# Kernel optimization log

Measured on AMD Instinct MI355X. Metric: run time of the kernel, lower is better.

Reference implementation:

```python
import jax, jax.numpy as jnp
import numpy as np

N_NODES = 20000
N_EDGES = 160000
N_GRAPHS = 64
DIMS = [9, 128, 256, 512, 1534]
NEG_SLOPE_ATT = 0.2   # GATConv attention LeakyReLU
NEG_SLOPE_ACT = 0.01  # nn.LeakyReLU between layers
EPS = 1e-5            # GraphNorm eps


def setup_inputs() -> dict:
    key = jax.random.key(0)
    inp = {}
    k, key = jax.random.split(key)
    inp['x'] = jax.random.normal(k, (N_NODES, DIMS[0]), jnp.float32)
    k, key = jax.random.split(key)
    inp['edge_index'] = jax.random.randint(k, (2, N_EDGES), 0, N_NODES)
    k, key = jax.random.split(key)
    inp['batch'] = jnp.sort(jax.random.randint(k, (N_NODES,), 0, N_GRAPHS))
    for l in range(4):
        din, dout = DIMS[l], DIMS[l + 1]
        k1, k2, k3, key = jax.random.split(key, 4)
        s = 1.0 / np.sqrt(din)
        inp[f'W{l}'] = (jax.random.normal(k1, (din, dout)) * s).astype(jnp.float32)
        inp[f'asrc{l}'] = (jax.random.normal(k2, (dout,)) * 0.1).astype(jnp.float32)
        inp[f'adst{l}'] = (jax.random.normal(k3, (dout,)) * 0.1).astype(jnp.float32)
        inp[f'b{l}'] = jnp.zeros((dout,), jnp.float32)
        inp[f'g{l}'] = jnp.ones((dout,), jnp.float32)   # GraphNorm weight
        inp[f'bt{l}'] = jnp.zeros((dout,), jnp.float32)  # GraphNorm bias
        inp[f'ms{l}'] = jnp.ones((dout,), jnp.float32)   # GraphNorm mean_scale
    return inp


def _gat_conv(h, src, dst, n, W, asrc, adst, b):
    # PyG GATConv, heads=1: linear (no bias), edge attention, segment softmax, scatter-add
    hp = h @ W                                                    # [N, dout]
    e = jax.nn.leaky_relu((hp @ asrc)[src] + (hp @ adst)[dst], NEG_SLOPE_ATT)  # [E]
    m = jax.ops.segment_max(e, dst, num_segments=n)
    m = jnp.where(jnp.isfinite(m), m, 0.0)
    ex = jnp.exp(e - m[dst])
    denom = jax.ops.segment_sum(ex, dst, num_segments=n)
    alpha = ex / (denom[dst] + 1e-16)                             # [E]
    out = jax.ops.segment_sum(alpha[:, None] * hp[src], dst, num_segments=n)
    return out + b


def _graph_norm(h, batch, counts, g, bt, ms):
    # PyG GraphNorm: per-graph mean/var with learnable mean_scale
    mean = jax.ops.segment_sum(h, batch, num_segments=N_GRAPHS) / counts
    out = h - ms * mean[batch]
    var = jax.ops.segment_sum(out * out, batch, num_segments=N_GRAPHS) / counts
    return out / jnp.sqrt(var[batch] + EPS) * g + bt


def _forward(x, edge_index, batch, params):
    n = x.shape[0]
    loops = jnp.arange(n)
    src = jnp.concatenate([edge_index[0], loops])   # GATConv add_self_loops=True
    dst = jnp.concatenate([edge_index[1], loops])
    counts = jax.ops.segment_sum(jnp.ones((n,), x.dtype), batch, num_segments=N_GRAPHS)[:, None]
    h = x
    for (W, asrc, adst, b, g, bt, ms) in params:
        h = _gat_conv(h, src, dst, n, W, asrc, adst, b)
        h = jax.nn.leaky_relu(h, NEG_SLOPE_ACT)
        h = _graph_norm(h, batch, counts, g, bt, ms)
        # Dropout(p=0.1) is identity in eval mode
    mean = (jax.ops.segment_sum(h, batch, num_segments=N_GRAPHS) / counts)[:, None, :]
    mx = jax.ops.segment_max(h, batch, num_segments=N_GRAPHS)[:, None, :]
    return jnp.concatenate([mean, mx], axis=1)      # [G, 2, 1534]


def reference(x, edge_index, batch,
              W0, asrc0, adst0, b0, g0, bt0, ms0,
              W1, asrc1, adst1, b1, g1, bt1, ms1,
              W2, asrc2, adst2, b2, g2, bt2, ms2,
              W3, asrc3, adst3, b3, g3, bt3, ms3):
    params = [
        (W0, asrc0, adst0, b0, g0, bt0, ms0),
        (W1, asrc1, adst1, b1, g1, bt1, ms1),
        (W2, asrc2, adst2, b2, g2, bt2, ms2),
        (W3, asrc3, adst3, b3, g3, bt3, ms3),
    ]
    return _forward(x, edge_index, batch, params)
```

## Files before the change

### kernel.cpp

```cpp
#include <hip/hip_runtime.h>
#include <math.h>

typedef unsigned int u32;
typedef unsigned short u16;
using half8 = __attribute__((ext_vector_type(8))) _Float16;
using f32x4 = __attribute__((ext_vector_type(4))) float;

#define NN 20000
#define MPAD 20096
#define NE 160000
#define ET 180000
#define NG 64
#define NBLK 79

constexpr float NEG_ATT = 0.2f;
constexpr float NEG_ACT = 0.01f;
constexpr float EPS_GN  = 1e-5f;

struct Ptr4 { const float *p0, *p1, *p2, *p3; };


__device__ __forceinline__ u16 f2h(float f) {
    _Float16 h = (_Float16)f;
    return __builtin_bit_cast(u16, h);
}
__device__ __forceinline__ float h2f(u16 b) {
    return (float)__builtin_bit_cast(_Float16, b);
}

__device__ __forceinline__ void gl_lds16(const void* g, void* l) {
    __builtin_amdgcn_global_load_lds((const __attribute__((address_space(1))) u32*)g,
                                     (__attribute__((address_space(3))) u32*)l, 16, 0, 0);
}

__device__ __forceinline__ float lrelu_att(float v) {
    return (v > 0.f) ? v : NEG_ATT * v;
}


__global__ void k_bounds(const int* __restrict__ batch, int* __restrict__ counts,
                         int* __restrict__ gstart) {
    __shared__ int ls[NG + 1];
    int g = threadIdx.x;
    int lo = 0, hi = NN;
    while (lo < hi) {
        int mid = (lo + hi) >> 1;
        if (batch[mid] < g) lo = mid + 1; else hi = mid;
    }
    ls[g] = lo;
    if (g == 0) ls[NG] = NN;
    __syncthreads();
    counts[g] = ls[g + 1] - ls[g];
    gstart[g] = ls[g];
    if (g == 0) gstart[NG] = NN;
}


__global__ void k_deg(const int* __restrict__ ei, int* deg) {
    int i = blockIdx.x * 256 + threadIdx.x;
    if (i >= ET) return;
    int dst = (i < NE) ? ei[NE + i] : (i - NE);
    atomicAdd(&deg[dst], 1);
}

__global__ void k_scan1(const int* __restrict__ deg, int* __restrict__ bsum) {
    int i = blockIdx.x * 256 + threadIdx.x;
    int v = (i < NN) ? deg[i] : 0;
    int lane = threadIdx.x & 63, w = threadIdx.x >> 6;
    #pragma unroll
    for (int off = 32; off; off >>= 1) v += __shfl_down(v, off, 64);
    __shared__ int ws[4];
    if (lane == 0) ws[w] = v;
    __syncthreads();
    if (threadIdx.x == 0) bsum[blockIdx.x] = ws[0] + ws[1] + ws[2] + ws[3];
}

__global__ void k_scan2(const int* __restrict__ bsum, int* __restrict__ boff,
                        int* __restrict__ total) {
    int tid = threadIdx.x;
    int v = (tid < NBLK) ? bsum[tid] : 0;
    int lane = tid & 63, w = tid >> 6;
    int val = v;
    #pragma unroll
    for (int off = 1; off < 64; off <<= 1) {
        int t = __shfl_up(val, off, 64);
        if (lane >= off) val += t;
    }
    __shared__ int ws[4];
    if (lane == 63) ws[w] = val;
    __syncthreads();
    int woff = 0;
    for (int k = 0; k < w; k++) woff += ws[k];
    int excl = woff + val - v;
    if (tid < NBLK) boff[tid] = excl;
    if (tid == NBLK - 1) *total = excl + v;
}

__global__ void k_scan3(const int* __restrict__ deg, const int* __restrict__ boff,
                        int* __restrict__ row_ptr, int* __restrict__ cursor) {
    int i = blockIdx.x * 256 + threadIdx.x;
    int v = (i < NN) ? deg[i] : 0;
    int lane = threadIdx.x & 63, w = threadIdx.x >> 6;
    int val = v;
    #pragma unroll
    for (int off = 1; off < 64; off <<= 1) {
        int t = __shfl_up(val, off, 64);
        if (lane >= off) val += t;
    }
    __shared__ int ws[4];
    if (lane == 63) ws[w] = val;
    __syncthreads();
    int woff = 0;
    for (int k = 0; k < w; k++) woff += ws[k];
    int excl = boff[blockIdx.x] + woff + val - v;
    if (i < NN) { row_ptr[i] = excl; cursor[i] = excl; }
}

__global__ void k_scatter(const int* __restrict__ ei, int* cursor, int* __restrict__ col) {
    int i = blockIdx.x * 256 + threadIdx.x;
    if (i >= ET) return;
    int s, d;
    if (i < NE) { s = ei[i]; d = ei[NE + i]; } else { s = i - NE; d = s; }
    int p = atomicAdd(&cursor[d], 1);
    col[p] = s;
}


__global__ void k_wvec_all(Ptr4 W, Ptr4 As, Ptr4 Ad,
                           float* __restrict__ wsrcA, float* __restrict__ wdstA) {
    const int dins[4]  = {9, 128, 256, 512};
    const int douts[4] = {128, 256, 512, 1534};
    int l = blockIdx.y, k = blockIdx.x;
    if (k >= dins[l]) return;
    const float* Wp = (l == 0) ? W.p0 : (l == 1) ? W.p1 : (l == 2) ? W.p2 : W.p3;
    const float* as = (l == 0) ? As.p0 : (l == 1) ? As.p1 : (l == 2) ? As.p2 : As.p3;
    const float* ad = (l == 0) ? Ad.p0 : (l == 1) ? Ad.p1 : (l == 2) ? Ad.p2 : Ad.p3;
    int NC = douts[l];
    const float* row = Wp + (size_t)k * NC;
    float ss = 0.f, sd = 0.f;
    for (int n = threadIdx.x; n < NC; n += 256) {
        float w = row[n];
        ss += w * as[n];
        sd += w * ad[n];
    }
    __shared__ float ls[8];
    int lane = threadIdx.x & 63, w4 = threadIdx.x >> 6;
    #pragma unroll
    for (int off = 32; off; off >>= 1) {
        ss += __shfl_down(ss, off, 64);
        sd += __shfl_down(sd, off, 64);
    }
    if (lane == 0) { ls[w4] = ss; ls[4 + w4] = sd; }
    __syncthreads();
    if (threadIdx.x == 0) {
        wsrcA[l * 512 + k] = ls[0] + ls[1] + ls[2] + ls[3];
        wdstA[l * 512 + k] = ls[4] + ls[5] + ls[6] + ls[7];
    }
}


__global__ void k_wbt_all(Ptr4 W, u16* __restrict__ WbTall) {
    const int Ks[3] = {128, 256, 512};
    const int NCs[3] = {256, 512, 1534};
    const int Nps[3] = {256, 512, 1536};
    const size_t offs[3] = {0, 256 * 128, 256 * 128 + 512 * 256};
    int l = blockIdx.z;
    int K = Ks[l], NC = NCs[l], Np = Nps[l];
    int n0 = blockIdx.x * 32, k0 = blockIdx.y * 32;
    if (n0 >= Np || k0 >= K) return;
    const float* Wp = (l == 0) ? W.p1 : (l == 1) ? W.p2 : W.p3;
    u16* WbT = WbTall + offs[l];
    __shared__ u16 tile[32][33];
    int tx = threadIdx.x & 31, ty = threadIdx.x >> 5;
    #pragma unroll
    for (int i = 0; i < 4; i++) {
        int k = k0 + ty + i * 8, n = n0 + tx;
        float v = (k < K && n < NC) ? Wp[(size_t)k * NC + n] : 0.f;
        tile[ty + i * 8][tx] = f2h(v);
    }
    __syncthreads();
    #pragma unroll
    for (int i = 0; i < 4; i++) {
        int n = n0 + ty + i * 8, k = k0 + tx;
        if (n < Np && k < K) WbT[(size_t)n * K + k] = tile[tx][ty + i * 8];
    }
}


__global__ void k_scores0(const float* __restrict__ x, const float* __restrict__ wsrc,
                          const float* __restrict__ wdst, float* __restrict__ s_src,
                          float* __restrict__ s_dst) {
    int v = blockIdx.x * 256 + threadIdx.x;
    if (v >= NN) return;
    const float* r = x + (size_t)v * 9;
    float ss = 0.f, sd = 0.f;
    #pragma unroll
    for (int k = 0; k < 9; k++) { ss += r[k] * wsrc[k]; sd += r[k] * wdst[k]; }
    s_src[v] = ss; s_dst[v] = sd;
}

template <int VW>
__global__ void k_scores_h(const u16* __restrict__ h, const float* __restrict__ wsrc,
                           const float* __restrict__ wdst, float* __restrict__ s_src,
                           float* __restrict__ s_dst, int din) {
    int v = blockIdx.x * 4 + (threadIdx.x >> 6);
    int lane = threadIdx.x & 63;
    if (v >= NN) return;
    const u16* row = h + (size_t)v * din;
    float ss = 0.f, sd = 0.f;
    for (int d = lane * VW; d < din; d += 64 * VW) {
        u32 ua[VW / 2];
        if constexpr (VW == 2) {
            ua[0] = *(const u32*)(row + d);
        } else if constexpr (VW == 4) {
            uint2 t = *(const uint2*)(row + d);
            ua[0] = t.x; ua[1] = t.y;
        } else {
            uint4 t = *(const uint4*)(row + d);
            ua[0] = t.x; ua[1] = t.y; ua[2] = t.z; ua[3] = t.w;
        }
        #pragma unroll
        for (int j = 0; j < VW / 2; j++) {
            float h0 = h2f((u16)(ua[j] & 0xffffu)), h1 = h2f((u16)(ua[j] >> 16));
            ss += h0 * wsrc[d + 2 * j] + h1 * wsrc[d + 2 * j + 1];
            sd += h0 * wdst[d + 2 * j] + h1 * wdst[d + 2 * j + 1];
        }
    }
    #pragma unroll
    for (int off = 32; off; off >>= 1) {
        ss += __shfl_down(ss, off, 64);
        sd += __shfl_down(sd, off, 64);
    }
    if (lane == 0) { s_src[v] = ss; s_dst[v] = sd; }
}


__global__ __launch_bounds__(256) void k_alpha(const int* __restrict__ row_ptr,
                                               const int* __restrict__ col,
                                               const float* __restrict__ s_src,
                                               const float* __restrict__ s_dst,
                                               float* __restrict__ alpha) {
    int grp = threadIdx.x >> 6;
    int lane = threadIdx.x & 63;
    int v = blockIdx.x * 4 + grp;
    if (v >= NN) return;
    int st = row_ptr[v], en = row_ptr[v + 1];
    float sd = s_dst[v];
    float mx = -INFINITY;
    for (int p = st + lane; p < en; p += 64)
        mx = fmaxf(mx, lrelu_att(s_src[col[p]] + sd));
    #pragma unroll
    for (int off = 32; off; off >>= 1) mx = fmaxf(mx, __shfl_xor(mx, off, 64));
    float sum = 0.f;
    for (int p = st + lane; p < en; p += 64)
        sum += __expf(lrelu_att(s_src[col[p]] + sd) - mx);
    #pragma unroll
    for (int off = 32; off; off >>= 1) sum += __shfl_xor(sum, off, 64);
    float inv = 1.0f / (sum + 1e-16f);
    for (int p = st + lane; p < en; p += 64)
        alpha[p] = __expf(lrelu_att(s_src[col[p]] + sd) - mx) * inv;
}


template <int TPN, int CPT>
__global__ __launch_bounds__(256) void k_agg2(const u16* __restrict__ h,
                                              const int* __restrict__ row_ptr,
                                              const int* __restrict__ col,
                                              const float* __restrict__ alpha,
                                              u16* __restrict__ agg, int din) {
    constexpr int NPB = 256 / TPN;
    int grp = threadIdx.x / TPN;
    int lane = threadIdx.x % TPN;
    int v = blockIdx.x * NPB + grp;
    if (v >= NN) return;
    int st = row_ptr[v], en = row_ptr[v + 1];
    int d0 = lane * 2 * CPT;
    const u16* hb = h + d0;
    float acc[2 * CPT];
    #pragma unroll
    for (int i = 0; i < 2 * CPT; i++) acc[i] = 0.f;

    auto ld = [&](int c, u32* t) {
        if constexpr (CPT == 1) {
            t[0] = *(const u32*)(hb + (size_t)c * din);
        } else if constexpr (CPT == 2) {
            uint2 u = *(const uint2*)(hb + (size_t)c * din);
            t[0] = u.x; t[1] = u.y;
        } else {
            uint4 u = *(const uint4*)(hb + (size_t)c * din);
            t[0] = u.x; t[1] = u.y; t[2] = u.z; t[3] = u.w;
        }
    };

    int p = st;
    for (; p + 4 <= en; p += 4) {
        float aa[4];
        u32 t[4][CPT];
        #pragma unroll
        for (int e = 0; e < 4; e++) {
            int c = col[p + e];
            aa[e] = alpha[p + e];
            ld(c, t[e]);
        }
        #pragma unroll
        for (int e = 0; e < 4; e++)
            #pragma unroll
            for (int j = 0; j < CPT; j++) {
                acc[2 * j]     += aa[e] * h2f((u16)(t[e][j] & 0xffffu));
                acc[2 * j + 1] += aa[e] * h2f((u16)(t[e][j] >> 16));
            }
    }
    for (; p < en; p++) {
        float a = alpha[p];
        u32 t[CPT];
        ld(col[p], t);
        #pragma unroll
        for (int j = 0; j < CPT; j++) {
            acc[2 * j]     += a * h2f((u16)(t[j] & 0xffffu));
            acc[2 * j + 1] += a * h2f((u16)(t[j] >> 16));
        }
    }

    u32 o[CPT];
    #pragma unroll
    for (int j = 0; j < CPT; j++)
        o[j] = (u32)f2h(acc[2 * j]) | ((u32)f2h(acc[2 * j + 1]) << 16);
    if constexpr (CPT == 1) {
        *(u32*)(agg + (size_t)v * din + d0) = o[0];
    } else if constexpr (CPT == 2) {
        uint2 ov; ov.x = o[0]; ov.y = o[1];
        *(uint2*)(agg + (size_t)v * din + d0) = ov;
    } else {
        uint4 ov; ov.x = o[0]; ov.y = o[1]; ov.z = o[2]; ov.w = o[3];
        *(uint4*)(agg + (size_t)v * din + d0) = ov;
    }
}

__global__ __launch_bounds__(256) void k_agg0_fused(const float* __restrict__ x,
                                                    const int* __restrict__ row_ptr,
                                                    const int* __restrict__ col,
                                                    const float* __restrict__ s_src,
                                                    const float* __restrict__ s_dst,
                                                    float* __restrict__ agg0) {
    __shared__ float sm[4 * 2];
    int grp = threadIdx.x >> 6;
    int lane = threadIdx.x & 63;
    int v = blockIdx.x * 4 + grp;
    bool valid = v < NN;
    int st = 0, en = 0;
    float sd = 0.f;
    if (valid) { st = row_ptr[v]; en = row_ptr[v + 1]; sd = s_dst[v]; }
    float mx = -INFINITY;
    if (valid) {
        for (int p = st + lane; p < en; p += 64)
            mx = fmaxf(mx, lrelu_att(s_src[col[p]] + sd));
    }
    #pragma unroll
    for (int off = 32; off; off >>= 1) mx = fmaxf(mx, __shfl_xor(mx, off, 64));
    float sum = 0.f;
    if (valid) {
        for (int p = st + lane; p < en; p += 64)
            sum += __expf(lrelu_att(s_src[col[p]] + sd) - mx);
    }
    #pragma unroll
    for (int off = 32; off; off >>= 1) sum += __shfl_xor(sum, off, 64);
    if (lane == 0) { sm[grp * 2] = mx; sm[grp * 2 + 1] = 1.0f / (sum + 1e-16f); }
    __syncthreads();
    if (!valid || lane >= 9) return;
    float m = sm[grp * 2], inv = sm[grp * 2 + 1];
    float acc = 0.f;
    for (int p = st; p < en; p++) {
        int c = col[p];
        float a = __expf(lrelu_att(s_src[c] + sd) - m);
        acc += a * x[(size_t)c * 9 + lane];
    }
    agg0[(size_t)v * 9 + lane] = acc * inv;
}


__global__ __launch_bounds__(256) void k_gemm0(const float* __restrict__ agg0,
                                               const float* __restrict__ W,
                                               const float* __restrict__ bias,
                                               u16* __restrict__ out) {
    __shared__ float Ws[9 * 128];
    for (int i = threadIdx.x; i < 9 * 128; i += 256) Ws[i] = W[i];
    __syncthreads();
    int node = blockIdx.x * 2 + (threadIdx.x >> 7);
    int n = threadIdx.x & 127;
    if (node >= NN) return;
    const float* xr = agg0 + (size_t)node * 9;
    float acc = bias[n];
    #pragma unroll
    for (int k = 0; k < 9; k++) acc += xr[k] * Ws[k * 128 + n];
    acc = (acc > 0.f) ? acc : NEG_ACT * acc;
    out[(size_t)node * 128 + n] = f2h(acc);
}


#define BM 128
#define BK 32

__global__ __launch_bounds__(256) void k_gemm_f16(const u16* __restrict__ A,
                                                  const u16* __restrict__ B,
                                                  const float* __restrict__ bias,
                                                  u16* __restrict__ C,
                                                  int K, int ldC, int NC, int ntx) {
    int nwg = gridDim.x;
    int b = blockIdx.x;
    int q = nwg >> 3, r = nwg & 7;
    int xcd = b & 7, idx = b >> 3;
    int wg = (xcd < r ? xcd * (q + 1) : r * (q + 1) + (xcd - r) * q) + idx;
    int row0 = (wg / ntx) * BM;
    int col0 = (wg % ntx) * BM;

    __shared__ u16 lds[2][2][BM * BK];
    int tid = threadIdx.x;
    int lane = tid & 63, w = tid >> 6;
    int wr = w >> 1, wc = w & 1;

    f32x4 acc[4][4];
    #pragma unroll
    for (int m = 0; m < 4; m++)
        #pragma unroll
        for (int n = 0; n < 4; n++)
            #pragma unroll
            for (int rr2 = 0; rr2 < 4; rr2++) acc[m][n][rr2] = 0.f;

    int nt = K / BK;

    auto stage = [&](int buf, int t) {
        int k0 = t * BK;
        #pragma unroll
        for (int c = 0; c < 2; c++) {
            int idx2 = tid + c * 256;
            int rr2 = idx2 >> 2, kc = idx2 & 3;
            int kcs = kc ^ (rr2 & 3);
            gl_lds16(A + (size_t)(row0 + rr2) * K + k0 + kcs * 8, &lds[buf][0][idx2 * 8]);
            gl_lds16(B + (size_t)(col0 + rr2) * K + k0 + kcs * 8, &lds[buf][1][idx2 * 8]);
        }
    };

    auto compute = [&](int buf) {
        const u16* As = &lds[buf][0][0];
        const u16* Bs = &lds[buf][1][0];
        int kg = lane >> 4, rl = lane & 15;
        half8 af[4], bfr[4];
        #pragma unroll
        for (int m = 0; m < 4; m++) {
            int rr2 = wr * 64 + m * 16 + rl;
            af[m] = *(const half8*)(As + rr2 * BK + (kg ^ (rr2 & 3)) * 8);
        }
        #pragma unroll
        for (int n = 0; n < 4; n++) {
            int rr2 = wc * 64 + n * 16 + rl;
            bfr[n] = *(const half8*)(Bs + rr2 * BK + (kg ^ (rr2 & 3)) * 8);
        }
        #pragma unroll
        for (int m = 0; m < 4; m++)
            #pragma unroll
            for (int n = 0; n < 4; n++)
                acc[m][n] = __builtin_amdgcn_mfma_f32_16x16x32_f16(af[m], bfr[n], acc[m][n], 0, 0, 0);
    };

    stage(0, 0);
    __syncthreads();
    for (int t = 0; t < nt; t++) {
        if (t + 1 < nt) stage((t + 1) & 1, t + 1);
        compute(t & 1);
        __syncthreads();
    }

    u16* ep = ((u16*)lds) + w * (32 * 72);
    int kg = lane >> 4, rl = lane & 15;
    int rrow = lane >> 3;
    int c8 = (lane & 7) * 8;
    #pragma unroll
    for (int half = 0; half < 2; half++) {
        #pragma unroll
        for (int m2 = 0; m2 < 2; m2++) {
            int m = half * 2 + m2;
            #pragma unroll
            for (int n = 0; n < 4; n++) {
                int colg = col0 + wc * 64 + n * 16 + rl;
                float bb = (colg < NC) ? bias[colg] : 0.f;
                #pragma unroll
                for (int rr2 = 0; rr2 < 4; rr2++) {
                    float o = acc[m][n][rr2] + bb;
                    o = (o > 0.f) ? o : NEG_ACT * o;
                    ep[(m2 * 16 + kg * 4 + rr2) * 72 + n * 16 + rl] = f2h(o);
                }
            }
        }
        #pragma unroll
        for (int it = 0; it < 4; it++) {
            int rloc = it * 8 + rrow;
            half8 vv = *(const half8*)(ep + rloc * 72 + c8);
            int rowg = row0 + wr * 64 + half * 32 + rloc;
            *(half8*)(C + (size_t)rowg * ldC + col0 + wc * 64 + c8) = vv;
        }
    }
}


__global__ __launch_bounds__(1024, 4) void k_gemm256(const u16* __restrict__ A,
                                                     const u16* __restrict__ B,
                                                     const float* __restrict__ bias,
                                                     u16* __restrict__ C,
                                                     int K, int ldC, int NC, int ntx, int M) {
    __shared__ u16 sMem[49152];

    int nwg = gridDim.x, b = blockIdx.x;
    int q = nwg >> 3, r = nwg & 7;
    int xcd = b & 7, bidx = b >> 3;
    int wg = (xcd < r ? xcd * (q + 1) : r * (q + 1) + (xcd - r) * q) + bidx;
    int row0 = (wg / ntx) * 256;
    int col0 = (wg % ntx) * 256;

    int tid = threadIdx.x;
    int w = tid >> 6, lane = tid & 63;
    int wm = w >> 2, wn = w & 3;
    int rl = lane & 15, kg = lane >> 4;
    int ksl = (kg ^ ((rl >> 1) & 3)) * 8;

    f32x4 acc[4][4];
    #pragma unroll
    for (int m = 0; m < 4; m++)
        #pragma unroll
        for (int n = 0; n < 4; n++)
            #pragma unroll
            for (int i = 0; i < 4; i++) acc[m][n][i] = 0.f;

    {
        int rr = tid >> 2, s = tid & 3;
        int ss = s ^ ((rr >> 1) & 3);
        int ra = row0 + rr; ra = (ra < M) ? ra : (M - 1);
        const u16* aSrc0 = A + (size_t)ra * K + ss * 8;
        const u16* bSrc0 = B + (size_t)(col0 + rr) * K + ss * 8;
        u16* dstA = sMem + tid * 8;
        u16* dstB = sMem + 8192 + tid * 8;

        auto stage = [&](int t, int bf2) {
            gl_lds16(aSrc0 + t * 32, dstA + bf2 * 16384);
            gl_lds16(bSrc0 + t * 32, dstB + bf2 * 16384);
        };

        half8 af[4], bf[4];
        auto ldAB = [&](int bf2) {
            const u16* Ab = sMem + bf2 * 16384;
            const u16* Bb = Ab + 8192;
            #pragma unroll
            for (int i = 0; i < 4; i++)
                af[i] = *(const half8*)(Ab + (wm * 64 + i * 16 + rl) * 32 + ksl);
            #pragma unroll
            for (int i = 0; i < 4; i++)
                bf[i] = *(const half8*)(Bb + (wn * 64 + i * 16 + rl) * 32 + ksl);
        };

        int nt = K >> 5;

        stage(0, 0); stage(1, 1);
        __builtin_amdgcn_sched_barrier(0);
        asm volatile("s_waitcnt vmcnt(2)" ::: "memory");
        __builtin_amdgcn_s_barrier();
        __builtin_amdgcn_sched_barrier(0);

        int rb = 0;
        for (int t = 0; t < nt; t++) {
            int sb = rb + 2; if (sb >= 3) sb -= 3;
            if (t + 2 < nt) stage(t + 2, sb);
            ldAB(rb);
            __builtin_amdgcn_s_setprio(1);
            #pragma unroll
            for (int i = 0; i < 4; i++)
                #pragma unroll
                for (int n = 0; n < 4; n++)
                    acc[i][n] = __builtin_amdgcn_mfma_f32_16x16x32_f16(af[i], bf[n], acc[i][n], 0, 0, 0);
            __builtin_amdgcn_s_setprio(0);
            __builtin_amdgcn_sched_barrier(0);
            if (t + 2 < nt)      asm volatile("s_waitcnt vmcnt(2)" ::: "memory");
            else if (t + 1 < nt) asm volatile("s_waitcnt vmcnt(0)" ::: "memory");
            __builtin_amdgcn_s_barrier();
            __builtin_amdgcn_sched_barrier(0);
            rb = (rb == 2) ? 0 : rb + 1;
        }
    }

    u16* ep = sMem + w * (32 * 72);
    float bv[4];
    #pragma unroll
    for (int n = 0; n < 4; n++) {
        int colg = col0 + wn * 64 + n * 16 + rl;
        bv[n] = (colg < NC) ? bias[colg] : 0.f;
    }
    int rrow = lane >> 3, c8 = (lane & 7) * 8;
    #pragma unroll
    for (int mh = 0; mh < 2; mh++) {
        #pragma unroll
        for (int msub = 0; msub < 2; msub++) {
            int m = mh * 2 + msub;
            #pragma unroll
            for (int n = 0; n < 4; n++) {
                #pragma unroll
                for (int rg = 0; rg < 4; rg++) {
                    float o = acc[m][n][rg] + bv[n];
                    o = (o > 0.f) ? o : NEG_ACT * o;
                    ep[(msub * 16 + kg * 4 + rg) * 72 + n * 16 + rl] = f2h(o);
                }
            }
        }
        #pragma unroll
        for (int it = 0; it < 4; it++) {
            int rloc = it * 8 + rrow;
            half8 vv = *(const half8*)(ep + rloc * 72 + c8);
            int rowg = row0 + wm * 64 + mh * 32 + rloc;
            if (rowg < M)
                *(half8*)(C + (size_t)rowg * ldC + col0 + wn * 64 + c8) = vv;
        }
    }
}


__global__ __launch_bounds__(256) void k_gn_fused(const u16* __restrict__ h,
                           const int* __restrict__ gstart,
                           const float* __restrict__ ms, const float* __restrict__ gam,
                           const float* __restrict__ bet, u16* __restrict__ out, int ld) {
    int g = blockIdx.x;
    int c0 = blockIdx.y * 128;
    int ct = threadIdx.x & 15, rg = threadIdx.x >> 4;
    int d0 = c0 + ct * 8;
    int st = gstart[g], en = gstart[g + 1];
    float inv = 1.0f / (float)(en - st);
    float s[8], qq[8];
    #pragma unroll
    for (int i = 0; i < 8; i++) { s[i] = 0.f; qq[i] = 0.f; }
    for (int r = st + rg; r < en; r += 16) {
        uint4 u = *(const uint4*)(h + (size_t)r * ld + d0);
        u32 ua[4] = {u.x, u.y, u.z, u.w};
        #pragma unroll
        for (int j = 0; j < 4; j++) {
            float v0 = h2f((u16)(ua[j] & 0xffffu)), v1 = h2f((u16)(ua[j] >> 16));
            s[2 * j] += v0; s[2 * j + 1] += v1;
            qq[2 * j] += v0 * v0; qq[2 * j + 1] += v1 * v1;
        }
    }
    __shared__ float Ls[16][128], Lq[16][128];
    #pragma unroll
    for (int i = 0; i < 8; i++) { Ls[rg][ct * 8 + i] = s[i]; Lq[rg][ct * 8 + i] = qq[i]; }
    __syncthreads();
    int tid = threadIdx.x;
    if (tid < 128) {
        float ss = 0.f, sq = 0.f;
        #pragma unroll
        for (int r2 = 1; r2 < 16; r2++) { ss += Ls[r2][tid]; sq += Lq[r2][tid]; }
        Ls[0][tid] += ss; Lq[0][tid] += sq;
    }
    __syncthreads();
    float sub[8], sc[8], bv[8];
    #pragma unroll
    for (int i = 0; i < 8; i++) {
        int cl = ct * 8 + i, d = d0 + i;
        float msv = ms[d];
        float mean = Ls[0][cl] * inv;
        float q2   = Lq[0][cl] * inv;
        float var  = fmaxf(q2 - (2.f * msv - msv * msv) * mean * mean, 0.f);
        sub[i] = msv * mean;
        sc[i]  = gam[d] * rsqrtf(var + EPS_GN);
        bv[i]  = bet[d];
    }
    for (int r = st + rg; r < en; r += 16) {
        uint4 u = *(const uint4*)(h + (size_t)r * ld + d0);
        u32 ua[4] = {u.x, u.y, u.z, u.w};
        uint4 wv4;
        u32 wo[4];
        #pragma unroll
        for (int j = 0; j < 4; j++) {
            float o0 = (h2f((u16)(ua[j] & 0xffffu)) - sub[2 * j]) * sc[2 * j] + bv[2 * j];
            float o1 = (h2f((u16)(ua[j] >> 16)) - sub[2 * j + 1]) * sc[2 * j + 1] + bv[2 * j + 1];
            wo[j] = (u32)f2h(o0) | ((u32)f2h(o1) << 16);
        }
        wv4.x = wo[0]; wv4.y = wo[1]; wv4.z = wo[2]; wv4.w = wo[3];
        *(uint4*)(out + (size_t)r * ld + d0) = wv4;
    }
}


__global__ __launch_bounds__(256) void k_gn_poolf(const u16* __restrict__ h,
                           const int* __restrict__ gstart,
                           const float* __restrict__ ms, const float* __restrict__ gam,
                           const float* __restrict__ bet, float* __restrict__ out,
                           int dout, int ld) {
    int g = blockIdx.x;
    int c0 = blockIdx.y * 128;
    int ct = threadIdx.x & 15, rg = threadIdx.x >> 4;
    int d0 = c0 + ct * 8;
    int st = gstart[g], en = gstart[g + 1];
    float inv = 1.0f / (float)(en - st);
    float s[8], qq[8], mn[8], mx[8];
    #pragma unroll
    for (int i = 0; i < 8; i++) { s[i] = 0.f; qq[i] = 0.f; mn[i] = INFINITY; mx[i] = -INFINITY; }
    for (int r = st + rg; r < en; r += 16) {
        uint4 u = *(const uint4*)(h + (size_t)r * ld + d0);
        u32 ua[4] = {u.x, u.y, u.z, u.w};
        #pragma unroll
        for (int j = 0; j < 4; j++) {
            float v0 = h2f((u16)(ua[j] & 0xffffu)), v1 = h2f((u16)(ua[j] >> 16));
            s[2 * j] += v0; s[2 * j + 1] += v1;
            qq[2 * j] += v0 * v0; qq[2 * j + 1] += v1 * v1;
            mn[2 * j] = fminf(mn[2 * j], v0); mn[2 * j + 1] = fminf(mn[2 * j + 1], v1);
            mx[2 * j] = fmaxf(mx[2 * j], v0); mx[2 * j + 1] = fmaxf(mx[2 * j + 1], v1);
        }
    }
    __shared__ float Ls[16][128], Lq[16][128], Ln[16][128], Lx[16][128];
    #pragma unroll
    for (int i = 0; i < 8; i++) {
        Ls[rg][ct * 8 + i] = s[i]; Lq[rg][ct * 8 + i] = qq[i];
        Ln[rg][ct * 8 + i] = mn[i]; Lx[rg][ct * 8 + i] = mx[i];
    }
    __syncthreads();
    int tid = threadIdx.x;
    if (tid < 128) {
        float ss = 0.f, sq = 0.f, amn = INFINITY, amx = -INFINITY;
        #pragma unroll
        for (int r2 = 0; r2 < 16; r2++) {
            ss += Ls[r2][tid]; sq += Lq[r2][tid];
            amn = fminf(amn, Ln[r2][tid]); amx = fmaxf(amx, Lx[r2][tid]);
        }
        int d = c0 + tid;
        if (d < dout) {
            float msv = ms[d];
            float mean = ss * inv;
            float q2   = sq * inv;
            float var  = fmaxf(q2 - (2.f * msv - msv * msv) * mean * mean, 0.f);
            float sc   = gam[d] * rsqrtf(var + EPS_GN);
            float off  = bet[d] - msv * mean * sc;
            out[(size_t)g * 2 * dout + d] = (mean - msv * mean) * sc + bet[d];
            float mval = (sc >= 0.f) ? amx : amn;
            out[(size_t)g * 2 * dout + dout + d] = mval * sc + off;
        }
    }
}


extern "C" void kernel_launch(void* const* d_in, const int* in_sizes, int n_in,
                              void* d_out, int out_size, void* d_ws, size_t ws_size,
                              hipStream_t stream) {
    const float* x = (const float*)d_in[0];
    const int* ei = (const int*)d_in[1];
    const int* batch = (const int*)d_in[2];
    const float *Wl[4], *Asr[4], *Ads[4], *Bi[4], *Ga[4], *Be[4], *Ms[4];
    for (int l = 0; l < 4; l++) {
        int b = 3 + 7 * l;
        Wl[l]  = (const float*)d_in[b];
        Asr[l] = (const float*)d_in[b + 1];
        Ads[l] = (const float*)d_in[b + 2];
        Bi[l]  = (const float*)d_in[b + 3];
        Ga[l]  = (const float*)d_in[b + 4];
        Be[l]  = (const float*)d_in[b + 5];
        Ms[l]  = (const float*)d_in[b + 6];
    }

    char* ws = (char*)d_ws;
    size_t off = 0;
    auto alloc = [&](size_t bytes) -> char* {
        char* p = ws + off;
        off += (bytes + 255) & ~(size_t)255;
        return p;
    };
    u16*   actA   = (u16*)alloc((size_t)MPAD * 512 * 2);
    u16*   actB   = (u16*)alloc((size_t)MPAD * 1536 * 2);
    u16*   agg    = (u16*)alloc((size_t)MPAD * 512 * 2);
    float* agg0   = (float*)alloc((size_t)NN * 9 * 4);
    u16*   WbTall = (u16*)alloc((size_t)(256 * 128 + 512 * 256 + 1536 * 512) * 2);
    float* wsrcA  = (float*)alloc((size_t)4 * 512 * 4);
    float* wdstA  = (float*)alloc((size_t)4 * 512 * 4);
    float* s_src  = (float*)alloc((size_t)NN * 4);
    float* s_dst  = (float*)alloc((size_t)NN * 4);
    float* alpha  = (float*)alloc((size_t)ET * 4);
    int* row_ptr  = (int*)alloc((size_t)(NN + 1) * 4);
    int* cursor   = (int*)alloc((size_t)NN * 4);
    int* colA     = (int*)alloc((size_t)ET * 4);
    int* counts   = (int*)alloc((size_t)NG * 4);
    int* gstart   = (int*)alloc((size_t)(NG + 1) * 4);
    int* bsum     = (int*)alloc((size_t)NBLK * 4);
    int* boff     = (int*)alloc((size_t)NBLK * 4);

    char* zbase = ws + off;
    int* deg      = (int*)alloc((size_t)NN * 4);
    size_t zbytes = (size_t)((ws + off) - zbase);
    hipMemsetAsync(zbase, 0, zbytes, stream);

    k_bounds<<<1, 64, 0, stream>>>(batch, counts, gstart);
    k_deg<<<(ET + 255) / 256, 256, 0, stream>>>(ei, deg);
    k_scan1<<<NBLK, 256, 0, stream>>>(deg, bsum);
    k_scan2<<<1, 256, 0, stream>>>(bsum, boff, row_ptr + NN);
    k_scan3<<<NBLK, 256, 0, stream>>>(deg, boff, row_ptr, cursor);
    k_scatter<<<(ET + 255) / 256, 256, 0, stream>>>(ei, cursor, colA);

    Ptr4 Wp{Wl[0], Wl[1], Wl[2], Wl[3]};
    Ptr4 Ap{Asr[0], Asr[1], Asr[2], Asr[3]};
    Ptr4 Dp{Ads[0], Ads[1], Ads[2], Ads[3]};
    k_wvec_all<<<dim3(512, 4), 256, 0, stream>>>(Wp, Ap, Dp, wsrcA, wdstA);
    k_wbt_all<<<dim3(48, 16, 3), 256, 0, stream>>>(Wp, WbTall);

    const int dims[5] = {9, 128, 256, 512, 1534};
    const size_t wbtOffs[3] = {0, 256 * 128, 256 * 128 + 512 * 256};
    const int RT256 = (MPAD + 255) / 256;

    for (int l = 0; l < 4; l++) {
        int din = dims[l], dout = dims[l + 1];
        int ldo = (dout == 1534) ? 1536 : dout;
        const float* wsrc = wsrcA + l * 512;
        const float* wdst = wdstA + l * 512;

        if (l == 0) {
            k_scores0<<<(NN + 255) / 256, 256, 0, stream>>>(x, wsrc, wdst, s_src, s_dst);
            k_agg0_fused<<<(NN + 3) / 4, 256, 0, stream>>>(x, row_ptr, colA, s_src, s_dst, agg0);
            k_gemm0<<<(NN + 1) / 2, 256, 0, stream>>>(agg0, Wl[0], Bi[0], actB);
        } else {
            if (din == 128)
                k_scores_h<2><<<(NN + 3) / 4, 256, 0, stream>>>(actA, wsrc, wdst, s_src, s_dst, din);
            else if (din == 256)
                k_scores_h<4><<<(NN + 3) / 4, 256, 0, stream>>>(actA, wsrc, wdst, s_src, s_dst, din);
            else
                k_scores_h<8><<<(NN + 3) / 4, 256, 0, stream>>>(actA, wsrc, wdst, s_src, s_dst, din);
            k_alpha<<<(NN + 3) / 4, 256, 0, stream>>>(row_ptr, colA, s_src, s_dst, alpha);
            if (din == 128)
                k_agg2<64, 1><<<(NN + 3) / 4, 256, 0, stream>>>(actA, row_ptr, colA, alpha, agg, din);
            else if (din == 256)
                k_agg2<64, 2><<<(NN + 3) / 4, 256, 0, stream>>>(actA, row_ptr, colA, alpha, agg, din);
            else
                k_agg2<64, 4><<<(NN + 3) / 4, 256, 0, stream>>>(actA, row_ptr, colA, alpha, agg, din);
            if (l <= 2) {
                int ntx = ldo / 128;
                int nwg = ntx * (MPAD / 128);
                k_gemm_f16<<<nwg, 256, 0, stream>>>(agg, WbTall + wbtOffs[l - 1], Bi[l], actB,
                                                    din, ldo, dout, ntx);
            } else {
                int ntx = ldo / 256;
                int nwg = ntx * RT256;
                k_gemm256<<<nwg, 1024, 0, stream>>>(agg, WbTall + wbtOffs[l - 1], Bi[l], actB,
                                                    din, ldo, dout, ntx, MPAD);
            }
        }

        if (l < 3)
            k_gn_fused<<<dim3(NG, ldo / 128), 256, 0, stream>>>(actB, gstart,
                                                                Ms[l], Ga[l], Be[l], actA, ldo);
        else
            k_gn_poolf<<<dim3(NG, 12), 256, 0, stream>>>(actB, gstart,
                                                         Ms[3], Ga[3], Be[3], (float*)d_out,
                                                         1534, 1536);
    }
}
```

Measured before the change: 308.3 us.

## Fuse final GraphNorm pooling statistics into last GEMM epilogue via per-tile partials

The last-layer GEMM no longer writes the 20000x1536 fp16 activation. Its epilogue instead reduces per-graph sum, sum of squares, min and max for each 256-row tile, using the sorted batch ids, and writes these float4 partials. A small finalize kernel combines the partials per graph and applies the GraphNorm affine to produce the mean and max pooled outputs. This removes a large activation write and re-read, at the cost of extra epilogue reductions and LDS traffic. It assumes at most three graphs fall within any 256-row tile.

```diff
diff --git a/kernel.cpp b/kernel.cpp
--- a/kernel.cpp
+++ b/kernel.cpp
@@ -12,6 +12,7 @@
 #define ET 180000
 #define NG 64
 #define NBLK 79
+#define RT256 79
 
 constexpr float NEG_ATT = 0.2f;
 constexpr float NEG_ACT = 0.01f;
@@ -502,18 +503,20 @@
 }
 
 
-__global__ __launch_bounds__(1024, 4) void k_gemm256(const u16* __restrict__ A,
-                                                     const u16* __restrict__ B,
-                                                     const float* __restrict__ bias,
-                                                     u16* __restrict__ C,
-                                                     int K, int ldC, int NC, int ntx, int M) {
+__global__ __launch_bounds__(1024, 4) void k_gemm256p(const u16* __restrict__ A,
+                                                      const u16* __restrict__ B,
+                                                      const float* __restrict__ bias,
+                                                      const int* __restrict__ batch,
+                                                      float4* __restrict__ partials,
+                                                      int K, int NC, int ntx, int M) {
     __shared__ u16 sMem[49152];
 
     int nwg = gridDim.x, b = blockIdx.x;
     int q = nwg >> 3, r = nwg & 7;
     int xcd = b & 7, bidx = b >> 3;
     int wg = (xcd < r ? xcd * (q + 1) : r * (q + 1) + (xcd - r) * q) + bidx;
-    int row0 = (wg / ntx) * 256;
+    int br = wg / ntx;
+    int row0 = br * 256;
     int col0 = (wg % ntx) * 256;
 
     int tid = threadIdx.x;
@@ -585,38 +588,129 @@
         }
     }
 
-    u16* ep = sMem + w * (32 * 72);
+    __syncthreads();
+    int* batLds  = (int*)sMem;
+    float* Lst   = (float*)((char*)sMem + 1024);
+    if (tid < 256) {
+        int rg2 = row0 + tid;
+        batLds[tid] = (rg2 < NN) ? batch[rg2] : -1;
+    }
+    __syncthreads();
+    int gbase = batLds[0];
+
     float bv[4];
     #pragma unroll
     for (int n = 0; n < 4; n++) {
         int colg = col0 + wn * 64 + n * 16 + rl;
         bv[n] = (colg < NC) ? bias[colg] : 0.f;
     }
-    int rrow = lane >> 3, c8 = (lane & 7) * 8;
-    #pragma unroll
-    for (int mh = 0; mh < 2; mh++) {
-        #pragma unroll
-        for (int msub = 0; msub < 2; msub++) {
-            int m = mh * 2 + msub;
-            #pragma unroll
-            for (int n = 0; n < 4; n++) {
+
+    #pragma unroll
+    for (int n = 0; n < 4; n++) {
+        float s0 = 0.f, q0 = 0.f, n0 = INFINITY, x0 = -INFINITY;
+        float s1 = 0.f, q1 = 0.f, n1 = INFINITY, x1 = -INFINITY;
+        float s2 = 0.f, q2 = 0.f, n2 = INFINITY, x2 = -INFINITY;
+        int gF = batLds[wm * 64 + kg * 4];
+        int gL = batLds[wm * 64 + 48 + kg * 4 + 3];
+        if (gF == gL && gF >= 0) {
+            float s = 0.f, qv = 0.f, mn = INFINITY, mx = -INFINITY;
+            #pragma unroll
+            for (int mh = 0; mh < 2; mh++)
                 #pragma unroll
-                for (int rg = 0; rg < 4; rg++) {
-                    float o = acc[m][n][rg] + bv[n];
-                    o = (o > 0.f) ? o : NEG_ACT * o;
-                    ep[(msub * 16 + kg * 4 + rg) * 72 + n * 16 + rl] = f2h(o);
-                }
-            }
-        }
-        #pragma unroll
-        for (int it = 0; it < 4; it++) {
-            int rloc = it * 8 + rrow;
-            half8 vv = *(const half8*)(ep + rloc * 72 + c8);
-            int rowg = row0 + wm * 64 + mh * 32 + rloc;
-            if (rowg < M)
-                *(half8*)(C + (size_t)rowg * ldC + col0 + wn * 64 + c8) = vv;
-        }
-    }
+                for (int msub = 0; msub < 2; msub++)
+                    #pragma unroll
+                    for (int rg = 0; rg < 4; rg++) {
+                        float o = acc[mh * 2 + msub][n][rg] + bv[n];
+                        o = (o > 0.f) ? o : NEG_ACT * o;
+                        s += o; qv += o * o;
+                        mn = fminf(mn, o); mx = fmaxf(mx, o);
+                    }
+            int gl = gF - gbase;
+            if (gl == 0)      { s0 = s; q0 = qv; n0 = mn; x0 = mx; }
+            else if (gl == 1) { s1 = s; q1 = qv; n1 = mn; x1 = mx; }
+            else              { s2 = s; q2 = qv; n2 = mn; x2 = mx; }
+        } else {
+            #pragma unroll
+            for (int mh = 0; mh < 2; mh++)
+                #pragma unroll
+                for (int msub = 0; msub < 2; msub++)
+                    #pragma unroll
+                    for (int rg = 0; rg < 4; rg++) {
+                        int rloc = wm * 64 + mh * 32 + msub * 16 + kg * 4 + rg;
+                        int g = batLds[rloc];
+                        float o = acc[mh * 2 + msub][n][rg] + bv[n];
+                        o = (o > 0.f) ? o : NEG_ACT * o;
+                        int gl = g - gbase;
+                        if (g >= 0) {
+                            if (gl == 0)      { s0 += o; q0 += o * o; n0 = fminf(n0, o); x0 = fmaxf(x0, o); }
+                            else if (gl == 1) { s1 += o; q1 += o * o; n1 = fminf(n1, o); x1 = fmaxf(x1, o); }
+                            else if (gl == 2) { s2 += o; q2 += o * o; n2 = fminf(n2, o); x2 = fmaxf(x2, o); }
+                        }
+                    }
+        }
+        #pragma unroll
+        for (int off = 16; off <= 32; off <<= 1) {
+            s0 += __shfl_xor(s0, off, 64); q0 += __shfl_xor(q0, off, 64);
+            n0 = fminf(n0, __shfl_xor(n0, off, 64)); x0 = fmaxf(x0, __shfl_xor(x0, off, 64));
+            s1 += __shfl_xor(s1, off, 64); q1 += __shfl_xor(q1, off, 64);
+            n1 = fminf(n1, __shfl_xor(n1, off, 64)); x1 = fmaxf(x1, __shfl_xor(x1, off, 64));
+            s2 += __shfl_xor(s2, off, 64); q2 += __shfl_xor(q2, off, 64);
+            n2 = fminf(n2, __shfl_xor(n2, off, 64)); x2 = fmaxf(x2, __shfl_xor(x2, off, 64));
+        }
+        if (kg == 0) {
+            int cl = wn * 64 + n * 16 + rl;
+            float* L0 = Lst + ((wm * 3 + 0) * 4) * 256 + cl;
+            float* L1 = Lst + ((wm * 3 + 1) * 4) * 256 + cl;
+            float* L2 = Lst + ((wm * 3 + 2) * 4) * 256 + cl;
+            L0[0] = s0; L0[256] = q0; L0[512] = n0; L0[768] = x0;
+            L1[0] = s1; L1[256] = q1; L1[512] = n1; L1[768] = x1;
+            L2[0] = s2; L2[256] = q2; L2[512] = n2; L2[768] = x2;
+        }
+    }
+    __syncthreads();
+    if (tid < 768) {
+        int gl = tid >> 8, cl = tid & 255;
+        float s = 0.f, qv = 0.f, mn = INFINITY, mx = -INFINITY;
+        #pragma unroll
+        for (int wm2 = 0; wm2 < 4; wm2++) {
+            const float* L = Lst + ((wm2 * 3 + gl) * 4) * 256 + cl;
+            s += L[0]; qv += L[256];
+            mn = fminf(mn, L[512]); mx = fmaxf(mx, L[768]);
+        }
+        float4 pv; pv.x = s; pv.y = qv; pv.z = mn; pv.w = mx;
+        partials[(size_t)(br * 3 + gl) * 1536 + col0 + cl] = pv;
+    }
+}
+
+__global__ __launch_bounds__(256) void k_poolfin(const float4* __restrict__ partials,
+                           const int* __restrict__ gstart, const int* __restrict__ batch,
+                           const float* __restrict__ ms, const float* __restrict__ gam,
+                           const float* __restrict__ bet, float* __restrict__ out, int dout) {
+    int d = blockIdx.x * 256 + threadIdx.x;
+    if (d >= dout) return;
+    int g = blockIdx.y;
+    int st = gstart[g], en = gstart[g + 1];
+    int br0 = st >> 8, br1 = (en - 1) >> 8;
+    float s = 0.f, q = 0.f, mn = INFINITY, mx = -INFINITY;
+    for (int br = br0; br <= br1; br++) {
+        int gb = batch[br << 8];
+        int gl = g - gb;
+        if (gl >= 0 && gl < 3) {
+            float4 p = partials[(size_t)(br * 3 + gl) * 1536 + d];
+            s += p.x; q += p.y;
+            mn = fminf(mn, p.z); mx = fmaxf(mx, p.w);
+        }
+    }
+    float inv = 1.0f / (float)(en - st);
+    float msv = ms[d];
+    float mean = s * inv;
+    float q2 = q * inv;
+    float var = fmaxf(q2 - (2.f * msv - msv * msv) * mean * mean, 0.f);
+    float sc = gam[d] * rsqrtf(var + EPS_GN);
+    float off = bet[d] - msv * mean * sc;
+    out[(size_t)g * 2 * dout + d] = (mean - msv * mean) * sc + bet[d];
+    float mval = (sc >= 0.f) ? mx : mn;
+    out[(size_t)g * 2 * dout + dout + d] = mval * sc + off;
 }
 
 
@@ -680,63 +774,6 @@
         }
         wv4.x = wo[0]; wv4.y = wo[1]; wv4.z = wo[2]; wv4.w = wo[3];
         *(uint4*)(out + (size_t)r * ld + d0) = wv4;
-    }
-}
-
-
-__global__ __launch_bounds__(256) void k_gn_poolf(const u16* __restrict__ h,
-                           const int* __restrict__ gstart,
-                           const float* __restrict__ ms, const float* __restrict__ gam,
-                           const float* __restrict__ bet, float* __restrict__ out,
-                           int dout, int ld) {
-    int g = blockIdx.x;
-    int c0 = blockIdx.y * 128;
-    int ct = threadIdx.x & 15, rg = threadIdx.x >> 4;
-    int d0 = c0 + ct * 8;
-    int st = gstart[g], en = gstart[g + 1];
-    float inv = 1.0f / (float)(en - st);
-    float s[8], qq[8], mn[8], mx[8];
-    #pragma unroll
-    for (int i = 0; i < 8; i++) { s[i] = 0.f; qq[i] = 0.f; mn[i] = INFINITY; mx[i] = -INFINITY; }
-    for (int r = st + rg; r < en; r += 16) {
-        uint4 u = *(const uint4*)(h + (size_t)r * ld + d0);
-        u32 ua[4] = {u.x, u.y, u.z, u.w};
-        #pragma unroll
-        for (int j = 0; j < 4; j++) {
-            float v0 = h2f((u16)(ua[j] & 0xffffu)), v1 = h2f((u16)(ua[j] >> 16));
-            s[2 * j] += v0; s[2 * j + 1] += v1;
-            qq[2 * j] += v0 * v0; qq[2 * j + 1] += v1 * v1;
-            mn[2 * j] = fminf(mn[2 * j], v0); mn[2 * j + 1] = fminf(mn[2 * j + 1], v1);
-            mx[2 * j] = fmaxf(mx[2 * j], v0); mx[2 * j + 1] = fmaxf(mx[2 * j + 1], v1);
-        }
-    }
-    __shared__ float Ls[16][128], Lq[16][128], Ln[16][128], Lx[16][128];
-    #pragma unroll
-    for (int i = 0; i < 8; i++) {
-        Ls[rg][ct * 8 + i] = s[i]; Lq[rg][ct * 8 + i] = qq[i];
-        Ln[rg][ct * 8 + i] = mn[i]; Lx[rg][ct * 8 + i] = mx[i];
-    }
-    __syncthreads();
-    int tid = threadIdx.x;
-    if (tid < 128) {
-        float ss = 0.f, sq = 0.f, amn = INFINITY, amx = -INFINITY;
-        #pragma unroll
-        for (int r2 = 0; r2 < 16; r2++) {
-            ss += Ls[r2][tid]; sq += Lq[r2][tid];
-            amn = fminf(amn, Ln[r2][tid]); amx = fmaxf(amx, Lx[r2][tid]);
-        }
-        int d = c0 + tid;
-        if (d < dout) {
-            float msv = ms[d];
-            float mean = ss * inv;
-            float q2   = sq * inv;
-            float var  = fmaxf(q2 - (2.f * msv - msv * msv) * mean * mean, 0.f);
-            float sc   = gam[d] * rsqrtf(var + EPS_GN);
-            float off  = bet[d] - msv * mean * sc;
-            out[(size_t)g * 2 * dout + d] = (mean - msv * mean) * sc + bet[d];
-            float mval = (sc >= 0.f) ? amx : amn;
-            out[(size_t)g * 2 * dout + dout + d] = mval * sc + off;
-        }
     }
 }
 
@@ -767,7 +804,7 @@
         return p;
     };
     u16*   actA   = (u16*)alloc((size_t)MPAD * 512 * 2);
-    u16*   actB   = (u16*)alloc((size_t)MPAD * 1536 * 2);
+    u16*   actB   = (u16*)alloc((size_t)MPAD * 512 * 2);
     u16*   agg    = (u16*)alloc((size_t)MPAD * 512 * 2);
     float* agg0   = (float*)alloc((size_t)NN * 9 * 4);
     u16*   WbTall = (u16*)alloc((size_t)(256 * 128 + 512 * 256 + 1536 * 512) * 2);
@@ -776,6 +813,7 @@
     float* s_src  = (float*)alloc((size_t)NN * 4);
     float* s_dst  = (float*)alloc((size_t)NN * 4);
     float* alpha  = (float*)alloc((size_t)ET * 4);
+    float4* partials = (float4*)alloc((size_t)RT256 * 3 * 1536 * 16);
     int* row_ptr  = (int*)alloc((size_t)(NN + 1) * 4);
     int* cursor   = (int*)alloc((size_t)NN * 4);
     int* colA     = (int*)alloc((size_t)ET * 4);
@@ -804,7 +842,6 @@
 
     const int dims[5] = {9, 128, 256, 512, 1534};
     const size_t wbtOffs[3] = {0, 256 * 128, 256 * 128 + 512 * 256};
-    const int RT256 = (MPAD + 255) / 256;
 
     for (int l = 0; l < 4; l++) {
         int din = dims[l], dout = dims[l + 1];
@@ -838,8 +875,8 @@
             } else {
                 int ntx = ldo / 256;
                 int nwg = ntx * RT256;
-                k_gemm256<<<nwg, 1024, 0, stream>>>(agg, WbTall + wbtOffs[l - 1], Bi[l], actB,
-                                                    din, ldo, dout, ntx, MPAD);
+                k_gemm256p<<<nwg, 1024, 0, stream>>>(agg, WbTall + wbtOffs[l - 1], Bi[l],
+                                                     batch, partials, din, dout, ntx, MPAD);
             }
         }
 
@@ -847,8 +884,8 @@
             k_gn_fused<<<dim3(NG, ldo / 128), 256, 0, stream>>>(actB, gstart,
                                                                 Ms[l], Ga[l], Be[l], actA, ldo);
         else
-            k_gn_poolf<<<dim3(NG, 12), 256, 0, stream>>>(actB, gstart,
-                                                         Ms[3], Ga[3], Be[3], (float*)d_out,
-                                                         1534, 1536);
-    }
-}
+            k_poolfin<<<dim3(6, NG), 256, 0, stream>>>(partials, gstart, batch,
+                                                       Ms[3], Ga[3], Be[3],
+                                                       (float*)d_out, 1534);
+    }
+}
```

After: 316.5 us. +2.6%, slower.
